# Optimization experiments

Hardware: AMD Instinct MI355X
Metric: run time of the kernel (lower is better)

Reference implementation:

```python
import jax, jax.numpy as jnp
import numpy as np

B, M, D, K = 512, 32, 2048, 3
COUPLING_STRENGTH = 0.1
SPATIAL_DECAY = 2.0


def setup_inputs() -> dict:
    key = jax.random.key(0)
    k1, k2 = jax.random.split(key)
    x = jax.random.normal(k1, (B, M, D), dtype=jnp.float32)  # stacked module activities
    w = jax.random.normal(k2, (D, K), dtype=jnp.float32) * 0.1  # conv1d weight [out=D, in=1, K] squeezed
    return {"x": x, "w": w}


def reference(x, w):
    # x: [B, M, D] stacked module activities; w: [D, K] field-propagation conv weight.
    b, m, d = x.shape
    k = w.shape[1]
    pad = k // 2
    # Conv1d(in=1, out=D, padding=pad) followed by mean over the length dim is
    # exactly: E[b,m,c] = (1/D) * sum_k w[c,k] * S_k, where S_k is the sum of x
    # over the input positions actually touched by tap k (zero padding drops edges).
    T = x.sum(-1)                       # [B, M] total sum
    cs = jnp.cumsum(x, axis=-1)         # [B, M, D] prefix sums
    S_list = []
    for kk in range(k):                 # K is a small static constant
        o = kk - pad                    # tap offset; touched indices [max(0,o), D-1+min(0,o)]
        if o > 0:
            S_list.append(T - cs[..., o - 1])       # drop first o entries
        elif o < 0:
            S_list.append(cs[..., d - 1 + o])       # drop last |o| entries
        else:
            S_list.append(T)
    S = jnp.stack(S_list, axis=-1)      # [B, M, K]
    fields = jnp.einsum('bmk,dk->bmd', S, w) / d  # electric fields [B, M, D]
    # distance-decayed coupling with self-term excluded (i != j in the loop)
    idx = jnp.arange(m)
    decay = jnp.exp(-jnp.abs(idx[:, None] - idx[None, :]).astype(x.dtype) / SPATIAL_DECAY)
    decay = decay * (1.0 - jnp.eye(m, dtype=x.dtype))  # zero diagonal
    weighted = jnp.einsum('ij,bjd->bid', decay, fields)  # [B, M, D]
    return x + COUPLING_STRENGTH * weighted
```

## Files before the change

### kernel.cpp

```cpp
#include <hip/hip_runtime.h>
#include <stdint.h>

#define B_ 512
#define M_ 32
#define D_ 2048
#define Q4 128

typedef float fvec4 __attribute__((ext_vector_type(4)));

static __device__ __forceinline__ uint32_t pk_bf16(float lo, float hi) {
    uint32_t r;
    asm("v_cvt_pk_bf16_f32 %0, %1, %2" : "=v"(r) : "v"(lo), "v"(hi));
    return r;
}
static __device__ __forceinline__ float bf_lo(uint32_t u) { return __uint_as_float(u << 16); }
static __device__ __forceinline__ float bf_hi(uint32_t u) { return __uint_as_float(u & 0xFFFF0000u); }

static __device__ __forceinline__ void lds_barrier() {
    asm volatile("s_waitcnt lgkmcnt(0)" ::: "memory");
    __builtin_amdgcn_s_barrier();
}

__global__ __launch_bounds__(1024, 4) void ephaptic_pipe(const float* __restrict__ x,
                                                         const float* __restrict__ w,
                                                         float* __restrict__ out) {
    const int tid = threadIdx.x;
    const int b0 = blockIdx.x * 2;

    __shared__ uint32_t sx[4][M_][256];
    __shared__ float sT[M_], sF[M_], sL[M_];
    __shared__ fvec4 sCA[M_], sCB[M_];

    const int m = tid >> 5;
    const int t = tid & 31;
    const int p4 = tid & 127;
    const int rg = tid >> 7;

    const fvec4* wf = (const fvec4*)w;

    float psum = 0.f, first = 0.f, last = 0.f;
    fvec4 a0, a1, a2, a3;
    fvec4 e0, e1, e2, e3;

    auto RL = [&](int b, int rq, fvec4& v0, fvec4& v1, fvec4& v2, fvec4& v3) {
        const fvec4* row = (const fvec4*)(x + ((size_t)b * M_ + m) * (size_t)D_) + rq * Q4;
        v0 = row[t];  v1 = row[t + 32];  v2 = row[t + 64];  v3 = row[t + 96];
    };
    auto RS = [&](int rq, const fvec4& v0, const fvec4& v1, const fvec4& v2, const fvec4& v3) {
        psum += (v0.x+v0.y)+(v0.z+v0.w) + (v1.x+v1.y)+(v1.z+v1.w)
              + (v2.x+v2.y)+(v2.z+v2.w) + (v3.x+v3.y)+(v3.z+v3.w);
        if (rq == 0 && t == 0)  first = v0.x;
        if (rq == 3 && t == 31) last  = v3.w;
        uint2* sr = (uint2*)sx[rq][m];
        sr[t]      = make_uint2(pk_bf16(v0.x, v0.y), pk_bf16(v0.z, v0.w));
        sr[t + 32] = make_uint2(pk_bf16(v1.x, v1.y), pk_bf16(v1.z, v1.w));
        sr[t + 64] = make_uint2(pk_bf16(v2.x, v2.y), pk_bf16(v2.z, v2.w));
        sr[t + 96] = make_uint2(pk_bf16(v3.x, v3.y), pk_bf16(v3.z, v3.w));
    };
    auto SUMS = [&]() {
        float s = psum;
#pragma unroll
        for (int off = 16; off > 0; off >>= 1) s += __shfl_xor(s, off, 64);
        if (t == 0)  { sT[m] = s; sF[m] = first; }
        if (t == 31) { sL[m] = last; }
    };
    auto COEF = [&](fvec4* sC) {
        if (tid < M_) {
            const int i = tid;
            float r0 = 0.f, r1 = 0.f, r2 = 0.f;
            for (int j = 0; j < M_; ++j) {
                if (j == i) continue;
                const float dij = __expf(-0.5f * fabsf((float)(i - j)));
                const float T = sT[j];
                r0 += dij * (T - sL[j]);
                r1 += dij * T;
                r2 += dij * (T - sF[j]);
            }
            const float s = 0.1f / (float)D_;
            sC[i] = (fvec4){r0 * s, r1 * s, r2 * s, 0.f};
        }
    };
    auto W = [&](int b, int wq, const fvec4* sC) {
        const fvec4 w0 = wf[(wq * Q4 + p4) * 3 + 0];
        const fvec4 w1 = wf[(wq * Q4 + p4) * 3 + 1];
        const fvec4 w2 = wf[(wq * Q4 + p4) * 3 + 2];
        fvec4* ob = (fvec4*)(out + (size_t)b * M_ * D_) + wq * Q4 + p4;
#pragma unroll
        for (int rr = 0; rr < 4; ++rr) {
            const int r = rg * 4 + rr;
            const fvec4 c = sC[r];
            const uint2 u = ((const uint2*)sx[wq][r])[p4];
            fvec4 o;
            o.x = bf_lo(u.x) + c.x * w0.x + c.y * w0.y + c.z * w0.z;
            o.y = bf_hi(u.x) + c.x * w0.w + c.y * w1.x + c.z * w1.y;
            o.z = bf_lo(u.y) + c.x * w1.z + c.y * w1.w + c.z * w2.x;
            o.w = bf_hi(u.y) + c.x * w2.y + c.y * w2.z + c.z * w2.w;
            __builtin_nontemporal_store(o, ob + (size_t)r * 512);
        }
    };

    RL(b0, 0, a0, a1, a2, a3);
    RL(b0, 1, e0, e1, e2, e3);
    RS(0, a0, a1, a2, a3);  RL(b0, 2, a0, a1, a2, a3);
    RS(1, e0, e1, e2, e3);  RL(b0, 3, e0, e1, e2, e3);
    RS(2, a0, a1, a2, a3);
    RS(3, e0, e1, e2, e3);
    SUMS();
    lds_barrier();
    COEF(sCA);
    lds_barrier();

    RL(b0 + 1, 0, a0, a1, a2, a3);  W(b0, 0, sCA);  lds_barrier();
    RL(b0 + 1, 1, e0, e1, e2, e3);  W(b0, 1, sCA);  lds_barrier();
    psum = 0.f;
    RS(0, a0, a1, a2, a3);  RL(b0 + 1, 2, a0, a1, a2, a3);  W(b0, 2, sCA);  lds_barrier();
    RS(1, e0, e1, e2, e3);  RL(b0 + 1, 3, e0, e1, e2, e3);  W(b0, 3, sCA);  lds_barrier();
    RS(2, a0, a1, a2, a3);
    RS(3, e0, e1, e2, e3);
    SUMS();
    lds_barrier();
    COEF(sCB);
    lds_barrier();

    W(b0 + 1, 0, sCB);
    W(b0 + 1, 1, sCB);
    W(b0 + 1, 2, sCB);
    W(b0 + 1, 3, sCB);
}

extern "C" void kernel_launch(void* const* d_in, const int* in_sizes, int n_in,
                              void* d_out, int out_size, void* d_ws, size_t ws_size,
                              hipStream_t stream) {
    const float* x = (const float*)d_in[0];
    const float* w = (const float*)d_in[1];
    float* out = (float*)d_out;
    ephaptic_pipe<<<B_ / 2, 1024, 0, stream>>>(x, w, out);
}
```

Baseline: 47.26 us.

## Compute coupling coefficients redundantly per wave and drop a barrier phase

Coupling coefficients were computed by a single group of 32 threads and shared through LDS. Now every wave computes the four coefficients it needs and passes them between lanes with shuffles, which removes one barrier and the idle serial phase after each batch's sums. The pipeline is also reordered so the next batch's first loads are issued before that barrier and each write stage overlaps the following reduce stage. The cost is redundant exp and loop work in every wave, plus more registers held for the coefficients.

```diff
diff --git a/kernel.cpp b/kernel.cpp
--- a/kernel.cpp
+++ b/kernel.cpp
@@ -29,18 +29,19 @@
 
     __shared__ uint32_t sx[4][M_][256];
     __shared__ float sT[M_], sF[M_], sL[M_];
-    __shared__ fvec4 sCA[M_], sCB[M_];
 
     const int m = tid >> 5;
     const int t = tid & 31;
     const int p4 = tid & 127;
     const int rg = tid >> 7;
+    const int lane = tid & 63;
 
     const fvec4* wf = (const fvec4*)w;
 
     float psum = 0.f, first = 0.f, last = 0.f;
     fvec4 a0, a1, a2, a3;
     fvec4 e0, e1, e2, e3;
+    float cc[4][3];
 
     auto RL = [&](int b, int rq, fvec4& v0, fvec4& v1, fvec4& v2, fvec4& v3) {
         const fvec4* row = (const fvec4*)(x + ((size_t)b * M_ + m) * (size_t)D_) + rq * Q4;
@@ -64,23 +65,27 @@
         if (t == 0)  { sT[m] = s; sF[m] = first; }
         if (t == 31) { sL[m] = last; }
     };
-    auto COEF = [&](fvec4* sC) {
-        if (tid < M_) {
-            const int i = tid;
-            float r0 = 0.f, r1 = 0.f, r2 = 0.f;
-            for (int j = 0; j < M_; ++j) {
-                if (j == i) continue;
-                const float dij = __expf(-0.5f * fabsf((float)(i - j)));
-                const float T = sT[j];
-                r0 += dij * (T - sL[j]);
-                r1 += dij * T;
-                r2 += dij * (T - sF[j]);
-            }
-            const float s = 0.1f / (float)D_;
-            sC[i] = (fvec4){r0 * s, r1 * s, r2 * s, 0.f};
+    auto CO = [&]() {
+        const int i = rg * 4 + (lane & 3);
+        float r0 = 0.f, r1 = 0.f, r2 = 0.f;
+        for (int j = 0; j < M_; ++j) {
+            const float dij = (j == i) ? 0.f : __expf(-0.5f * fabsf((float)(i - j)));
+            const float T = sT[j];
+            r0 += dij * (T - sL[j]);
+            r1 += dij * T;
+            r2 += dij * (T - sF[j]);
+        }
+        const float s = 0.1f / (float)D_;
+        r0 *= s; r1 *= s; r2 *= s;
+#pragma unroll
+        for (int rr = 0; rr < 4; ++rr) {
+            const int src = (lane & ~3) | rr;
+            cc[rr][0] = __shfl(r0, src, 64);
+            cc[rr][1] = __shfl(r1, src, 64);
+            cc[rr][2] = __shfl(r2, src, 64);
         }
     };
-    auto W = [&](int b, int wq, const fvec4* sC) {
+    auto W = [&](int b, int wq) {
         const fvec4 w0 = wf[(wq * Q4 + p4) * 3 + 0];
         const fvec4 w1 = wf[(wq * Q4 + p4) * 3 + 1];
         const fvec4 w2 = wf[(wq * Q4 + p4) * 3 + 2];
@@ -88,13 +93,12 @@
 #pragma unroll
         for (int rr = 0; rr < 4; ++rr) {
             const int r = rg * 4 + rr;
-            const fvec4 c = sC[r];
             const uint2 u = ((const uint2*)sx[wq][r])[p4];
             fvec4 o;
-            o.x = bf_lo(u.x) + c.x * w0.x + c.y * w0.y + c.z * w0.z;
-            o.y = bf_hi(u.x) + c.x * w0.w + c.y * w1.x + c.z * w1.y;
-            o.z = bf_lo(u.y) + c.x * w1.z + c.y * w1.w + c.z * w2.x;
-            o.w = bf_hi(u.y) + c.x * w2.y + c.y * w2.z + c.z * w2.w;
+            o.x = bf_lo(u.x) + cc[rr][0] * w0.x + cc[rr][1] * w0.y + cc[rr][2] * w0.z;
+            o.y = bf_hi(u.x) + cc[rr][0] * w0.w + cc[rr][1] * w1.x + cc[rr][2] * w1.y;
+            o.z = bf_lo(u.y) + cc[rr][0] * w1.z + cc[rr][1] * w1.w + cc[rr][2] * w2.x;
+            o.w = bf_hi(u.y) + cc[rr][0] * w2.y + cc[rr][1] * w2.z + cc[rr][2] * w2.w;
             __builtin_nontemporal_store(o, ob + (size_t)r * 512);
         }
     };
@@ -106,26 +110,27 @@
     RS(2, a0, a1, a2, a3);
     RS(3, e0, e1, e2, e3);
     SUMS();
+    RL(b0 + 1, 0, a0, a1, a2, a3);
+    RL(b0 + 1, 1, e0, e1, e2, e3);
     lds_barrier();
-    COEF(sCA);
+    CO();
+    W(b0, 0);
     lds_barrier();
-
-    RL(b0 + 1, 0, a0, a1, a2, a3);  W(b0, 0, sCA);  lds_barrier();
-    RL(b0 + 1, 1, e0, e1, e2, e3);  W(b0, 1, sCA);  lds_barrier();
     psum = 0.f;
-    RS(0, a0, a1, a2, a3);  RL(b0 + 1, 2, a0, a1, a2, a3);  W(b0, 2, sCA);  lds_barrier();
-    RS(1, e0, e1, e2, e3);  RL(b0 + 1, 3, e0, e1, e2, e3);  W(b0, 3, sCA);  lds_barrier();
-    RS(2, a0, a1, a2, a3);
+    RS(0, a0, a1, a2, a3);  RL(b0 + 1, 2, a0, a1, a2, a3);  W(b0, 1);
+    lds_barrier();
+    RS(1, e0, e1, e2, e3);  RL(b0 + 1, 3, e0, e1, e2, e3);  W(b0, 2);
+    lds_barrier();
+    RS(2, a0, a1, a2, a3);  W(b0, 3);
+    lds_barrier();
     RS(3, e0, e1, e2, e3);
     SUMS();
     lds_barrier();
-    COEF(sCB);
-    lds_barrier();
-
-    W(b0 + 1, 0, sCB);
-    W(b0 + 1, 1, sCB);
-    W(b0 + 1, 2, sCB);
-    W(b0 + 1, 3, sCB);
+    CO();
+    W(b0 + 1, 0);
+    W(b0 + 1, 1);
+    W(b0 + 1, 2);
+    W(b0 + 1, 3);
 }
 
 extern "C" void kernel_launch(void* const* d_in, const int* in_sizes, int n_in,
```

New measurement: 53.71 us. 13.6% more time.
